# Performance work log

Hardware: AMD Instinct MI355X
Metric: run time of the kernel (lower is better)

Reference implementation:

```python
import jax, jax.numpy as jnp
import numpy as np

N = 100_000          # nodes
E = 3_200_000        # edges (avg degree 32)
IN, HID, OUT = 128, 64, 40
POWERS = [6, 8, 10]
MAXP = 10
LN_EPS = 1e-5


def setup_inputs() -> dict:
    key = jax.random.key(0)
    ks = jax.random.split(key, 8)
    x = jax.random.normal(ks[0], (N, IN), jnp.float32)
    edge_index = jax.random.randint(ks[1], (2, E), 0, N, dtype=jnp.int32)
    # params (torch Linear: y = x @ W + b with W stored [in, out] here)
    W1 = jax.random.normal(ks[2], (IN, HID), jnp.float32) / np.sqrt(IN)
    b1 = jnp.zeros((HID,), jnp.float32)
    # MixHopConv has Linear for every power 0..max(powers); only p in POWERS are used
    Wc = jax.random.normal(ks[3], (MAXP + 1, HID, HID), jnp.float32) / np.sqrt(HID)
    bc = jnp.zeros((MAXP + 1, HID), jnp.float32)
    W2 = jax.random.normal(ks[4], (HID * len(POWERS), OUT), jnp.float32) / np.sqrt(HID * len(POWERS))
    b2 = jnp.zeros((OUT,), jnp.float32)
    g1 = jnp.ones((HID,), jnp.float32); be1 = jnp.zeros((HID,), jnp.float32)
    g2 = jnp.ones((HID * len(POWERS),), jnp.float32); be2 = jnp.zeros((HID * len(POWERS),), jnp.float32)
    return dict(x=x, edge_index=edge_index, W1=W1, b1=b1, Wc=Wc, bc=bc,
                W2=W2, b2=b2, g1=g1, be1=be1, g2=g2, be2=be2)


def _layer_norm(h, g, b):
    mu = jnp.mean(h, axis=-1, keepdims=True)
    var = jnp.mean(jnp.square(h - mu), axis=-1, keepdims=True)
    return (h - mu) * jax.lax.rsqrt(var + LN_EPS) * g + b


def _gcn_norm(edge_index, n, dtype):
    # add self loops (fill 1), symmetric normalization D^-1/2 (A+I) D^-1/2
    loops = jnp.arange(n, dtype=edge_index.dtype)
    src = jnp.concatenate([edge_index[0], loops])
    dst = jnp.concatenate([edge_index[1], loops])
    w = jnp.ones(src.shape[0], dtype)
    deg = jax.ops.segment_sum(w, dst, num_segments=n)
    dis = jnp.where(deg > 0, jax.lax.rsqrt(deg), 0.0)
    norm = dis[src] * w * dis[dst]
    return src, dst, norm


def reference(x, edge_index, W1, b1, Wc, bc, W2, b2, g1, be1, g2, be2):
    n = x.shape[0]
    src, dst, norm = _gcn_norm(edge_index, n, x.dtype)

    def propagate(h):  # out[i] = sum_{(j->i)} norm_ij * h[j]
        return jax.ops.segment_sum(norm[:, None] * h[src], dst, num_segments=n)

    h = jax.nn.gelu(x @ W1 + b1, approximate=False)
    h = _layer_norm(h, g1, be1)
    # dropout is identity in eval mode

    # MixHop: propagate MAXP times, apply per-power linear at p in POWERS
    outs = {}
    if 0 in POWERS:
        outs[0] = h @ Wc[0] + bc[0]
    cur = h
    for j in range(1, MAXP + 1):
        cur = propagate(cur)
        if j in POWERS:
            outs[j] = cur @ Wc[j] + bc[j]
    h = jnp.concatenate([outs[p] for p in POWERS], axis=-1)

    h = jax.nn.gelu(h, approximate=False)
    h = _layer_norm(h, g2, be2)
    return h @ W2 + b2
```

## Files before the change

kernel.cpp:

```cpp
#include <hip/hip_runtime.h>

typedef _Float16 h16;
typedef _Float16 h16x8 __attribute__((ext_vector_type(8)));
typedef short short8 __attribute__((ext_vector_type(8)));
typedef float f32x4 __attribute__((ext_vector_type(4)));

__device__ __forceinline__ float bf2f(unsigned short u) {
    return __uint_as_float(((unsigned)u) << 16);
}
__device__ __forceinline__ unsigned short f2bf(float f) {
    unsigned x = __float_as_uint(f);
    unsigned r = x + 0x7fffu + ((x >> 16) & 1u);
    return (unsigned short)(r >> 16);
}
__device__ __forceinline__ float gelu_fast(float v) {
    float y = 0.7978845608f * (v + 0.044715f * v * v * v);
    float e = __expf(2.0f * y);
    float th = 1.0f - 2.0f * __builtin_amdgcn_rcpf(e + 1.0f);
    return 0.5f * v * (1.0f + th);
}

__device__ __forceinline__ float ldin(const void* p, size_t i, int isbf) {
    return isbf ? bf2f(((const unsigned short*)p)[i]) : ((const float*)p)[i];
}

#define LN_EPS 1e-5f
#define NBMAX 256
#define BCAP 16

__global__ void k_flag(const unsigned* __restrict__ g1w, int* __restrict__ flag) {
    if (blockIdx.x == 0 && threadIdx.x == 0)
        *flag = (g1w[0] == 0x3F803F80u) ? 1 : 0;
}

__global__ void k_bcnt(const int* __restrict__ dst, int* __restrict__ bcnt, int E) {
    __shared__ int c[NBMAX];
    int t = threadIdx.x;
    c[t] = 0;
    __syncthreads();
    int stride = gridDim.x * 256;
    for (int i = blockIdx.x * 256 + t; i < E; i += stride)
        atomicAdd(&c[dst[i] >> 9], 1);
    __syncthreads();
    if (c[t] > 0) atomicAdd(&bcnt[t], c[t]);
}

__global__ void k_bscan(const int* __restrict__ bcnt, int* __restrict__ bbase,
                        int* __restrict__ gtail, int NB) {
    __shared__ int sh[NBMAX];
    int t = threadIdx.x;
    int v = (t < NB) ? bcnt[t] : 0;
    sh[t] = v;
    __syncthreads();
    for (int s = 1; s < 256; s <<= 1) {
        int u = 0;
        if (t >= s) u = sh[t - s];
        __syncthreads();
        sh[t] += u;
        __syncthreads();
    }
    if (t < NB) { int e = sh[t] - v; bbase[t] = e; gtail[t] = e; }
    if (t == 0) bbase[NB] = sh[NBMAX - 1];
}

__global__ void k_bin(const int* __restrict__ src, const int* __restrict__ dst,
                      int* __restrict__ gtail, unsigned* __restrict__ stg, int E) {
    __shared__ int cnt[NBMAX];
    __shared__ unsigned buf[BCAP * NBMAX];
    int t = threadIdx.x;
    int nbatch = (E + 1023) >> 10;
    for (int batch = blockIdx.x; batch < nbatch; batch += gridDim.x) {
        cnt[t] = 0;
        __syncthreads();
        int base = batch << 10;
        int i0 = base + t * 4;
        int4 s4, d4;
        bool full = (i0 + 4 <= E);
        if (full) {
            s4 = *(const int4*)(src + i0);
            d4 = *(const int4*)(dst + i0);
        }
#pragma unroll
        for (int r = 0; r < 4; r++) {
            int i = i0 + r;
            int s, d;
            if (full) {
                s = ((const int*)&s4)[r]; d = ((const int*)&d4)[r];
            } else {
                if (i >= E) continue;
                s = src[i]; d = dst[i];
            }
            int b = d >> 9;
            unsigned pr = ((unsigned)(d & 511) << 23) | (unsigned)s;
            int p = atomicAdd(&cnt[b], 1);
            if (p < BCAP) buf[p * NBMAX + b] = pr;
            else {
                int gp = atomicAdd(&gtail[b], 1);
                stg[gp] = pr;
            }
        }
        __syncthreads();
        int c = cnt[t];
        if (c > BCAP) c = BCAP;
        if (c > 0) {
            int gb = atomicAdd(&gtail[t], c);
            for (int i = 0; i < c; i++) stg[gb + i] = buf[i * NBMAX + t];
        }
        __syncthreads();
    }
}

__global__ void k_build2(const unsigned* __restrict__ stg, const int* __restrict__ bbase,
                         int* __restrict__ offv, float* __restrict__ dis,
                         float* __restrict__ d2, float* __restrict__ idis,
                         int* __restrict__ csr, int N, int E, int NB) {
    __shared__ int cnt[512];
    __shared__ int sc[512];
    __shared__ int pos[512];
    int b = blockIdx.x, t = threadIdx.x;
    cnt[t] = 0; cnt[t + 256] = 0;
    __syncthreads();
    int beg = bbase[b], end = bbase[b + 1];
    for (int k = beg + t; k < end; k += 256)
        atomicAdd(&cnt[stg[k] >> 23], 1);
    __syncthreads();
    sc[t] = cnt[t]; sc[t + 256] = cnt[t + 256];
    pos[t] = 0; pos[t + 256] = 0;
    __syncthreads();
    for (int s = 1; s < 512; s <<= 1) {
        int u0 = 0, u1 = 0;
        if (t >= s) u0 = sc[t - s];
        if (t + 256 >= s) u1 = sc[t + 256 - s];
        __syncthreads();
        sc[t] += u0; sc[t + 256] += u1;
        __syncthreads();
    }
    int nb9 = b << 9;
#pragma unroll
    for (int ii = 0; ii < 2; ii++) {
        int i = t + ii * 256;
        int node = nb9 + i;
        if (node < N) {
            offv[node] = beg + sc[i] - cnt[i];
            float dp1 = (float)(cnt[i] + 1);
            dis[node] = rsqrtf(dp1);
            d2[node] = 1.0f / dp1;
            idis[node] = sqrtf(dp1);
        }
    }
    if (b == NB - 1 && t == 0) offv[N] = E;
    __syncthreads();
    for (int k = beg + t; k < end; k += 256) {
        unsigned pr = stg[k];
        int dl = (int)(pr >> 23);
        int p = beg + (sc[dl] - cnt[dl]) + atomicAdd(&pos[dl], 1);
        csr[p] = (int)(pr & 0x7FFFFFu);
    }
}

__global__ void k_in(const void* __restrict__ x, const void* __restrict__ W1,
                     const void* __restrict__ b1, const void* __restrict__ g1,
                     const void* __restrict__ be1, const float* __restrict__ dis,
                     h16* __restrict__ h, const int* __restrict__ flag, int N) {
    __shared__ __align__(16) short Bf[4][4][64][8];
    int isbf = *flag;
    int tid = threadIdx.x;
    for (int idx = tid; idx < 4 * 4 * 64; idx += 256) {
        int c = idx >> 8, t = (idx >> 6) & 3, ln = idx & 63;
        int quad = ln >> 4, col = t * 16 + (ln & 15);
#pragma unroll
        for (int j = 0; j < 8; j++) {
            int k = c * 32 + quad * 8 + j;
            Bf[c][t][ln][j] = (short)f2bf(ldin(W1, (size_t)k * 64 + col, isbf));
        }
    }
    __syncthreads();
    int lane = tid & 63, quad = lane >> 4, m15 = lane & 15;
    float bcol[4], gcol[4], ecol[4];
#pragma unroll
    for (int t = 0; t < 4; t++) {
        int col = t * 16 + m15;
        bcol[t] = ldin(b1, col, isbf);
        gcol[t] = ldin(g1, col, isbf);
        ecol[t] = ldin(be1, col, isbf);
    }
    int wave = blockIdx.x * 4 + (tid >> 6);
    int nwave = gridDim.x * 4;
    int ntile = (N + 15) >> 4;
    for (int tile = wave; tile < ntile; tile += nwave) {
        int m0 = tile << 4;
        int mrow = m0 + m15; if (mrow >= N) mrow = N - 1;
        f32x4 acc[4];
#pragma unroll
        for (int t = 0; t < 4; t++)
#pragma unroll
            for (int r = 0; r < 4; r++) acc[t][r] = 0.0f;
#pragma unroll
        for (int c = 0; c < 4; c++) {
            short8 a;
            if (isbf) {
                a = *(const short8*)((const unsigned short*)x + (size_t)mrow * 128 + c * 32 + quad * 8);
            } else {
                const float* xp = (const float*)x + (size_t)mrow * 128 + c * 32 + quad * 8;
#pragma unroll
                for (int j = 0; j < 8; j++) a[j] = (short)f2bf(xp[j]);
            }
#pragma unroll
            for (int t = 0; t < 4; t++) {
                short8 b = *(const short8*)(&Bf[c][t][lane][0]);
                acc[t] = __builtin_amdgcn_mfma_f32_16x16x32_bf16(a, b, acc[t], 0, 0, 0);
            }
        }
        float v[4][4];
        float s[4] = {0, 0, 0, 0}, q[4] = {0, 0, 0, 0};
#pragma unroll
        for (int t = 0; t < 4; t++)
#pragma unroll
            for (int r = 0; r < 4; r++) {
                float g = gelu_fast(acc[t][r] + bcol[t]);
                v[t][r] = g;
                s[r] += g; q[r] += g * g;
            }
#pragma unroll
        for (int o = 1; o < 16; o <<= 1)
#pragma unroll
            for (int r = 0; r < 4; r++) {
                s[r] += __shfl_xor(s[r], o, 64);
                q[r] += __shfl_xor(q[r], o, 64);
            }
#pragma unroll
        for (int r = 0; r < 4; r++) {
            int node = m0 + quad * 4 + r;
            if (node < N) {
                float mu = s[r] * (1.0f / 64.0f);
                float var = q[r] * (1.0f / 64.0f) - mu * mu;
                float rs = rsqrtf(var + LN_EPS);
                float dn = dis[node];
#pragma unroll
                for (int t = 0; t < 4; t++) {
                    float hv = (v[t][r] - mu) * rs * gcol[t] + ecol[t];
                    h[(size_t)node * 64 + t * 16 + m15] = (h16)(dn * hv);
                }
            }
        }
    }
}

__global__ void k_prop(const h16* __restrict__ cur, h16* __restrict__ nxt,
                       const int* __restrict__ offv, const int* __restrict__ csr,
                       const float* __restrict__ d2, int N) {
    int node = blockIdx.x * 4 + (threadIdx.x >> 6);
    if (node >= N) return;
    int lane = threadIdx.x & 63;
    int g = lane >> 3, q = lane & 7;
    h16x8 acc = {0, 0, 0, 0, 0, 0, 0, 0};
    int e = offv[node], end = offv[node + 1];
#pragma unroll 2
    for (; e + 8 <= end; e += 8) {
        int s = csr[e + g];
        acc += *(const h16x8*)(cur + (size_t)s * 64 + q * 8);
    }
    int r = end - e;
    if (g < r) {
        int s = csr[e + g];
        acc += *(const h16x8*)(cur + (size_t)s * 64 + q * 8);
    }
#pragma unroll
    for (int o = 8; o < 64; o <<= 1) {
        h16x8 other;
        int* ap = (int*)&acc;
        int* op = (int*)&other;
#pragma unroll
        for (int i = 0; i < 4; i++) op[i] = __shfl_xor(ap[i], o, 64);
        acc += other;
    }
    if (g == 0) {
        float dd = d2[node];
        h16x8 sv = *(const h16x8*)(cur + (size_t)node * 64 + q * 8);
        h16x8 o8;
#pragma unroll
        for (int i = 0; i < 8; i++) o8[i] = (h16)(dd * ((float)acc[i] + (float)sv[i]));
        *(h16x8*)(nxt + (size_t)node * 64 + q * 8) = o8;
    }
}

__global__ void k_pout(const h16* __restrict__ cur, const void* __restrict__ Wc,
                       const void* __restrict__ bc, const float* __restrict__ idis,
                       h16* __restrict__ hcat, const int* __restrict__ flag,
                       size_t woff, size_t boff, int seg, int N) {
    __shared__ __align__(16) h16 Bf[2][4][64][8];
    int isbf = *flag;
    int tid = threadIdx.x;
    for (int idx = tid; idx < 2 * 4 * 64; idx += 256) {
        int c = idx >> 8, t = (idx >> 6) & 3, ln = idx & 63;
        int quad = ln >> 4, col = t * 16 + (ln & 15);
#pragma unroll
        for (int j = 0; j < 8; j++) {
            int k = c * 32 + quad * 8 + j;
            Bf[c][t][ln][j] = (h16)ldin(Wc, woff + (size_t)k * 64 + col, isbf);
        }
    }
    __syncthreads();
    int lane = tid & 63, quad = lane >> 4, m15 = lane & 15;
    float bcol[4];
#pragma unroll
    for (int t = 0; t < 4; t++) bcol[t] = ldin(bc, boff + t * 16 + m15, isbf);
    int wave = blockIdx.x * 4 + (tid >> 6);
    int nwave = gridDim.x * 4;
    int ntile = (N + 15) >> 4;
    for (int tile = wave; tile < ntile; tile += nwave) {
        int m0 = tile << 4;
        int mrow = m0 + m15; if (mrow >= N) mrow = N - 1;
        f32x4 acc[4];
#pragma unroll
        for (int t = 0; t < 4; t++)
#pragma unroll
            for (int r = 0; r < 4; r++) acc[t][r] = 0.0f;
#pragma unroll
        for (int c = 0; c < 2; c++) {
            h16x8 a = *(const h16x8*)(cur + (size_t)mrow * 64 + c * 32 + quad * 8);
#pragma unroll
            for (int t = 0; t < 4; t++) {
                h16x8 b = *(const h16x8*)(&Bf[c][t][lane][0]);
                acc[t] = __builtin_amdgcn_mfma_f32_16x16x32_f16(a, b, acc[t], 0, 0, 0);
            }
        }
#pragma unroll
        for (int r = 0; r < 4; r++) {
            int node = m0 + quad * 4 + r;
            if (node < N) {
                float di = idis[node];
#pragma unroll
                for (int t = 0; t < 4; t++)
                    hcat[(size_t)node * 192 + seg * 64 + t * 16 + m15] =
                        (h16)(bcol[t] + di * acc[t][r]);
            }
        }
    }
}

__global__ void k_fin(const h16* __restrict__ hcat, const void* __restrict__ g2,
                      const void* __restrict__ be2, const void* __restrict__ W2,
                      const void* __restrict__ b2, void* __restrict__ out,
                      const int* __restrict__ flag, int N) {
    __shared__ __align__(16) h16 Bf[6][3][64][8];
    __shared__ float2 GB[192];
    __shared__ __align__(16) h16 Y[4][16][200];
    int isbf = *flag;
    int tid = threadIdx.x;
    for (int idx = tid; idx < 6 * 3 * 64; idx += 256) {
        int c = idx / 192, rem = idx % 192;
        int t = rem >> 6, ln = rem & 63;
        int quad = ln >> 4, col = t * 16 + (ln & 15);
#pragma unroll
        for (int j = 0; j < 8; j++) {
            int k = c * 32 + quad * 8 + j;
            float w = (col < 40) ? ldin(W2, (size_t)k * 40 + col, isbf) : 0.0f;
            Bf[c][t][ln][j] = (h16)w;
        }
    }
    for (int i = tid; i < 192; i += 256) {
        float2 gb; gb.x = ldin(g2, i, isbf); gb.y = ldin(be2, i, isbf);
        GB[i] = gb;
    }
    __syncthreads();
    int wv = tid >> 6;
    int lane = tid & 63, quad = lane >> 4, m15 = lane & 15;
    float b2v[3];
#pragma unroll
    for (int t = 0; t < 3; t++) {
        int col = t * 16 + m15;
        b2v[t] = (col < 40) ? ldin(b2, col, isbf) : 0.0f;
    }
    int wave = blockIdx.x * 4 + wv;
    int nwave = gridDim.x * 4;
    int ntile = (N + 15) >> 4;
    for (int tile = wave; tile < ntile; tile += nwave) {
        int m0 = tile << 4;
        int mrow = m0 + m15; if (mrow >= N) mrow = N - 1;
        const h16* hp = hcat + (size_t)mrow * 192 + quad * 48;
        float s = 0.0f, q = 0.0f;
#pragma unroll
        for (int u = 0; u < 6; u++) {
            h16x8 vv = *(const h16x8*)(hp + u * 8);
            h16x8 gv;
#pragma unroll
            for (int j = 0; j < 8; j++) {
                float g = gelu_fast((float)vv[j]);
                gv[j] = (h16)g;
                s += g; q += g * g;
            }
            *(h16x8*)(&Y[wv][m15][quad * 48 + u * 8]) = gv;
        }
        s += __shfl_xor(s, 16, 64); s += __shfl_xor(s, 32, 64);
        q += __shfl_xor(q, 16, 64); q += __shfl_xor(q, 32, 64);
        float mu = s * (1.0f / 192.0f);
        float var = q * (1.0f / 192.0f) - mu * mu;
        float rs = rsqrtf(var + LN_EPS);
        asm volatile("s_waitcnt lgkmcnt(0)" ::: "memory");
        f32x4 acc[3];
#pragma unroll
        for (int t = 0; t < 3; t++)
#pragma unroll
            for (int r = 0; r < 4; r++) acc[t][r] = 0.0f;
#pragma unroll
        for (int c = 0; c < 6; c++) {
            h16x8 raw = *(const h16x8*)(&Y[wv][m15][c * 32 + quad * 8]);
            h16x8 a;
#pragma unroll
            for (int j = 0; j < 8; j++) {
                int k = c * 32 + quad * 8 + j;
                float2 gb = GB[k];
                a[j] = (h16)(((float)raw[j] - mu) * rs * gb.x + gb.y);
            }
#pragma unroll
            for (int t = 0; t < 3; t++) {
                h16x8 b = *(const h16x8*)(&Bf[c][t][lane][0]);
                acc[t] = __builtin_amdgcn_mfma_f32_16x16x32_f16(a, b, acc[t], 0, 0, 0);
            }
        }
        asm volatile("" ::: "memory");
#pragma unroll
        for (int r = 0; r < 4; r++) {
            int node = m0 + quad * 4 + r;
            if (node < N) {
#pragma unroll
                for (int t = 0; t < 3; t++) {
                    int col = t * 16 + m15;
                    if (col < 40) {
                        float o = acc[t][r] + b2v[t];
                        if (isbf) ((unsigned short*)out)[(size_t)node * 40 + col] = f2bf(o);
                        else      ((float*)out)[(size_t)node * 40 + col] = o;
                    }
                }
            }
        }
    }
}

extern "C" void kernel_launch(void* const* d_in, const int* in_sizes, int n_in,
                              void* d_out, int out_size, void* d_ws, size_t ws_size,
                              hipStream_t stream) {
    const int IN = 128, HID = 64;
    const int N = in_sizes[0] / IN;
    const int E = in_sizes[1] / 2;
    const int NB = (N + 511) >> 9;

    const void* x   = d_in[0];
    const int*  ei  = (const int*)d_in[1];
    const void* W1  = d_in[2];
    const void* b1  = d_in[3];
    const void* Wc  = d_in[4];
    const void* bc  = d_in[5];
    const void* W2  = d_in[6];
    const void* b2  = d_in[7];
    const void* g1  = d_in[8];
    const void* be1 = d_in[9];
    const void* g2  = d_in[10];
    const void* be2 = d_in[11];

    char* ws = (char*)d_ws;
    size_t off = 0;
    auto take = [&](size_t bytes) -> char* {
        char* p = ws + off;
        off = (off + bytes + 255) & ~(size_t)255;
        return p;
    };
    int*   flag  = (int*)take(256);
    int*   bcnt  = (int*)take(NBMAX * 4);
    int*   bbase = (int*)take((NBMAX + 1) * 4);
    int*   gtail = (int*)take(NBMAX * 4);
    float* dis   = (float*)take((size_t)N * 4);
    float* d2    = (float*)take((size_t)N * 4);
    float* idis  = (float*)take((size_t)N * 4);
    int*   offv  = (int*)take((size_t)(N + 1) * 4);
    int*   csr   = (int*)take((size_t)E * 4);
    size_t unionSz = (size_t)E * 4 > (size_t)N * 384 ? (size_t)E * 4 : (size_t)N * 384;
    char*  uni   = take(unionSz);
    unsigned* stg = (unsigned*)uni;
    h16*   hcat  = (h16*)uni;
    h16*   hA    = (h16*)take((size_t)N * HID * 2);
    h16*   hB    = (h16*)take((size_t)N * HID * 2);

    hipMemsetAsync(bcnt, 0, NBMAX * 4, stream);

    const int* srcp = ei;
    const int* dstp = ei + E;
    int gNode = (N + 3) / 4;
    int gDense = 1563;

    k_flag<<<1, 64, 0, stream>>>((const unsigned*)g1, flag);
    k_bcnt<<<512, 256, 0, stream>>>(dstp, bcnt, E);
    k_bscan<<<1, 256, 0, stream>>>(bcnt, bbase, gtail, NB);
    k_bin<<<2048, 256, 0, stream>>>(srcp, dstp, gtail, stg, E);
    k_build2<<<NB, 256, 0, stream>>>(stg, bbase, offv, dis, d2, idis, csr, N, E, NB);

    k_in<<<gDense, 256, 0, stream>>>(x, W1, b1, g1, be1, dis, hA, flag, N);
    h16* cur = hA; h16* nxt = hB;
    int seg = 0;
    for (int j = 1; j <= 10; j++) {
        k_prop<<<gNode, 256, 0, stream>>>(cur, nxt, offv, csr, d2, N);
        h16* tmp = cur; cur = nxt; nxt = tmp;
        if (j == 6 || j == 8 || j == 10) {
            k_pout<<<gDense, 256, 0, stream>>>(cur, Wc, bc, idis, hcat, flag,
                                               (size_t)j * HID * HID, (size_t)j * HID,
                                               seg, N);
            seg++;
        }
    }
    k_fin<<<gDense, 256, 0, stream>>>(hcat, g2, be2, W2, b2, d_out, flag, N);
}
```

Before: 921.5 us.

## Replace atomic-tail binning with per-block count and column-scan partitioning

Edge binning by destination bucket now records per-block bucket counts, runs a per-bucket scan across the blocks to get exclusive write offsets, and then has each block scatter its edges using only shared-memory atomics. This drops the global atomicAdd on the tail counters and the shared staging buffer that the old k_bin used for each batch. The cost is one extra kernel launch (k_colscan) plus a count and offset table stored temporarily in the CSR buffer. Writes to the staging array are no longer coalesced in batches.

Measured after the change: 910.2 us. Within noise of the previous version (-1.2%).

```diff
diff --git a/kernel.cpp b/kernel.cpp
--- a/kernel.cpp
+++ b/kernel.cpp
@@ -26,27 +26,29 @@
 
 #define LN_EPS 1e-5f
 #define NBMAX 256
-#define BCAP 16
+#define NBLK 1024
 
 __global__ void k_flag(const unsigned* __restrict__ g1w, int* __restrict__ flag) {
     if (blockIdx.x == 0 && threadIdx.x == 0)
         *flag = (g1w[0] == 0x3F803F80u) ? 1 : 0;
 }
 
-__global__ void k_bcnt(const int* __restrict__ dst, int* __restrict__ bcnt, int E) {
+__global__ void k_bcnt(const int* __restrict__ dst, int* __restrict__ bcnt,
+                       int* __restrict__ cnts, int E, int chunk) {
     __shared__ int c[NBMAX];
-    int t = threadIdx.x;
+    int t = threadIdx.x, blk = blockIdx.x;
     c[t] = 0;
     __syncthreads();
-    int stride = gridDim.x * 256;
-    for (int i = blockIdx.x * 256 + t; i < E; i += stride)
+    int beg = blk * chunk;
+    int end = beg + chunk; if (end > E) end = E;
+    for (int i = beg + t; i < end; i += 256)
         atomicAdd(&c[dst[i] >> 9], 1);
     __syncthreads();
+    cnts[blk * NBMAX + t] = c[t];
     if (c[t] > 0) atomicAdd(&bcnt[t], c[t]);
 }
 
-__global__ void k_bscan(const int* __restrict__ bcnt, int* __restrict__ bbase,
-                        int* __restrict__ gtail, int NB) {
+__global__ void k_bscan(const int* __restrict__ bcnt, int* __restrict__ bbase, int NB) {
     __shared__ int sh[NBMAX];
     int t = threadIdx.x;
     int v = (t < NB) ? bcnt[t] : 0;
@@ -59,54 +61,53 @@
         sh[t] += u;
         __syncthreads();
     }
-    if (t < NB) { int e = sh[t] - v; bbase[t] = e; gtail[t] = e; }
+    if (t < NB) bbase[t] = sh[t] - v;
     if (t == 0) bbase[NB] = sh[NBMAX - 1];
 }
 
+__global__ void k_colscan(const int* __restrict__ cnts, const int* __restrict__ bbase,
+                          int* __restrict__ base) {
+    __shared__ int sh[256];
+    int b = blockIdx.x, t = threadIdx.x;
+    int v[NBLK / 256];
+    int s = 0;
+#pragma unroll
+    for (int j = 0; j < NBLK / 256; j++) {
+        v[j] = cnts[(size_t)(t * (NBLK / 256) + j) * NBMAX + b];
+        s += v[j];
+    }
+    sh[t] = s;
+    __syncthreads();
+    for (int st = 1; st < 256; st <<= 1) {
+        int u = 0;
+        if (t >= st) u = sh[t - st];
+        __syncthreads();
+        sh[t] += u;
+        __syncthreads();
+    }
+    int run = bbase[b] + (t == 0 ? 0 : sh[t - 1]);
+#pragma unroll
+    for (int j = 0; j < NBLK / 256; j++) {
+        base[(size_t)(t * (NBLK / 256) + j) * NBMAX + b] = run;
+        run += v[j];
+    }
+}
+
 __global__ void k_bin(const int* __restrict__ src, const int* __restrict__ dst,
-                      int* __restrict__ gtail, unsigned* __restrict__ stg, int E) {
-    __shared__ int cnt[NBMAX];
-    __shared__ unsigned buf[BCAP * NBMAX];
-    int t = threadIdx.x;
-    int nbatch = (E + 1023) >> 10;
-    for (int batch = blockIdx.x; batch < nbatch; batch += gridDim.x) {
-        cnt[t] = 0;
-        __syncthreads();
-        int base = batch << 10;
-        int i0 = base + t * 4;
-        int4 s4, d4;
-        bool full = (i0 + 4 <= E);
-        if (full) {
-            s4 = *(const int4*)(src + i0);
-            d4 = *(const int4*)(dst + i0);
-        }
-#pragma unroll
-        for (int r = 0; r < 4; r++) {
-            int i = i0 + r;
-            int s, d;
-            if (full) {
-                s = ((const int*)&s4)[r]; d = ((const int*)&d4)[r];
-            } else {
-                if (i >= E) continue;
-                s = src[i]; d = dst[i];
-            }
-            int b = d >> 9;
-            unsigned pr = ((unsigned)(d & 511) << 23) | (unsigned)s;
-            int p = atomicAdd(&cnt[b], 1);
-            if (p < BCAP) buf[p * NBMAX + b] = pr;
-            else {
-                int gp = atomicAdd(&gtail[b], 1);
-                stg[gp] = pr;
-            }
-        }
-        __syncthreads();
-        int c = cnt[t];
-        if (c > BCAP) c = BCAP;
-        if (c > 0) {
-            int gb = atomicAdd(&gtail[t], c);
-            for (int i = 0; i < c; i++) stg[gb + i] = buf[i * NBMAX + t];
-        }
-        __syncthreads();
+                      const int* __restrict__ base, unsigned* __restrict__ stg,
+                      int E, int chunk) {
+    __shared__ int loc[NBMAX];
+    int t = threadIdx.x, blk = blockIdx.x;
+    loc[t] = base[(size_t)blk * NBMAX + t];
+    __syncthreads();
+    int beg = blk * chunk;
+    int end = beg + chunk; if (end > E) end = E;
+    for (int i = beg + t; i < end; i += 256) {
+        int s = src[i], d = dst[i];
+        int b = d >> 9;
+        unsigned pr = ((unsigned)(d & 511) << 23) | (unsigned)s;
+        int p = atomicAdd(&loc[b], 1);
+        stg[p] = pr;
     }
 }
 
@@ -445,6 +446,7 @@
     const int N = in_sizes[0] / IN;
     const int E = in_sizes[1] / 2;
     const int NB = (N + 511) >> 9;
+    const int chunk = (E + NBLK - 1) / NBLK;
 
     const void* x   = d_in[0];
     const int*  ei  = (const int*)d_in[1];
@@ -469,7 +471,6 @@
     int*   flag  = (int*)take(256);
     int*   bcnt  = (int*)take(NBMAX * 4);
     int*   bbase = (int*)take((NBMAX + 1) * 4);
-    int*   gtail = (int*)take(NBMAX * 4);
     float* dis   = (float*)take((size_t)N * 4);
     float* d2    = (float*)take((size_t)N * 4);
     float* idis  = (float*)take((size_t)N * 4);
@@ -481,6 +482,8 @@
     h16*   hcat  = (h16*)uni;
     h16*   hA    = (h16*)take((size_t)N * HID * 2);
     h16*   hB    = (h16*)take((size_t)N * HID * 2);
+    int*   cnts  = csr;
+    int*   base  = csr + (size_t)NBLK * NBMAX;
 
     hipMemsetAsync(bcnt, 0, NBMAX * 4, stream);
 
@@ -490,9 +493,10 @@
     int gDense = 1563;
 
     k_flag<<<1, 64, 0, stream>>>((const unsigned*)g1, flag);
-    k_bcnt<<<512, 256, 0, stream>>>(dstp, bcnt, E);
-    k_bscan<<<1, 256, 0, stream>>>(bcnt, bbase, gtail, NB);
-    k_bin<<<2048, 256, 0, stream>>>(srcp, dstp, gtail, stg, E);
+    k_bcnt<<<NBLK, 256, 0, stream>>>(dstp, bcnt, cnts, E, chunk);
+    k_bscan<<<1, 256, 0, stream>>>(bcnt, bbase, NB);
+    k_colscan<<<NB, 256, 0, stream>>>(cnts, bbase, base);
+    k_bin<<<NBLK, 256, 0, stream>>>(srcp, dstp, base, stg, E, chunk);
     k_build2<<<NB, 256, 0, stream>>>(stg, bbase, offv, dis, d2, idis, csr, N, E, NB);
 
     k_in<<<gDense, 256, 0, stream>>>(x, W1, b1, g1, be1, dis, hA, flag, N);
```
